# Optimization experiments

Hardware: AMD Instinct MI355X
Metric: run time of the kernel (lower is better)

Reference implementation:

```python
import jax, jax.numpy as jnp
import numpy as np


def setup_inputs() -> dict:
    key = jax.random.key(0)
    ks = jax.random.split(key, 10)
    B, S, I, Hy, H = 16, 4096, 256, 64, 512
    sc = 0.05
    return {
        "x": jax.random.normal(ks[0], (B, S, I), jnp.float32),
        "hidden": jax.random.normal(ks[1], (B, H), jnp.float32),
        "lin0_W": jax.random.normal(ks[2], (Hy, I), jnp.float32) * sc,
        "lin0_b": jax.random.normal(ks[3], (Hy,), jnp.float32) * sc,
        "sig0_W": jax.random.normal(ks[4], (Hy, I), jnp.float32) * sc,
        "sig0_b": jax.random.normal(ks[5], (Hy,), jnp.float32) * sc,
        "fch_W": jax.random.normal(ks[6], (H, Hy), jnp.float32) * sc,
        "fch_b": jax.random.normal(ks[7], (H,), jnp.float32) * sc,
        "fc2_W": jax.random.normal(ks[8], (H, I), jnp.float32) * sc,
        "fc2_b": jax.random.normal(ks[9], (H,), jnp.float32) * sc,
    }


def reference(x, hidden, lin0_W, lin0_b, sig0_W, sig0_b, fch_W, fch_b, fc2_W, fc2_b):
    # GLN sub-network (num_layers=1): relu(linear(x) * sigmoid(linear(x)))
    lin = jnp.einsum('bsi,hi->bsh', x, lin0_W) + lin0_b          # [B,S,Hy]
    gate = jax.nn.sigmoid(jnp.einsum('bsi,hi->bsh', x, sig0_W) + sig0_b)
    g = jax.nn.relu(lin * gate)                                   # [B,S,Hy]
    b = jnp.einsum('bsh,dh->bsd', g, fch_W) + fch_b               # [B,S,H]
    # multihead gating
    sig_alphas = jax.nn.sigmoid(jnp.einsum('bsi,di->bsd', x, fc2_W) + fc2_b)
    b = b * sig_alphas

    # sequential recurrence: h_t = relu(b_t + roll(h_{t-1}, 1, -1)); h_{-1} = hidden
    def step(h, b_t):
        h = jax.nn.relu(b_t + jnp.roll(h, 1, axis=-1))
        return h, h

    b_tmajor = jnp.swapaxes(b, 0, 1)  # [S,B,H]
    last, outs = jax.lax.scan(step, hidden, b_tmajor)
    outputs = jnp.swapaxes(outs, 0, 1)  # [B,S,H]
    return outputs, last
```

## Files before the change

### kernel.cpp

```cpp
#include <hip/hip_runtime.h>

typedef __attribute__((ext_vector_type(4))) float  f32x4;
typedef __attribute__((ext_vector_type(4))) short  s16x4;
typedef __attribute__((ext_vector_type(8))) short  s16x8;
typedef __bf16 bf16x8 __attribute__((ext_vector_type(8)));

#define NBATCH 16
#define SEQ    4096
#define KIN    256
#define HY     64
#define HOUT   512
#define NROWS  (NBATCH*SEQ)
#define LC     32
#define NC     (SEQ/LC)

#define GP(x) ((const __attribute__((address_space(1))) void*)(x))
#define LP(x) ((__attribute__((address_space(3))) void*)(x))

static __device__ __forceinline__ short f2bf(float f) {
  unsigned u = __float_as_uint(f);
  u = u + 0x7FFF + ((u >> 16) & 1);
  return (short)(u >> 16);
}
static __device__ __forceinline__ float bf2f(short h) {
  return __uint_as_float(((unsigned)(unsigned short)h) << 16);
}
static __device__ __forceinline__ f32x4 mfma16(bf16x8 a, bf16x8 b, f32x4 c) {
  return __builtin_amdgcn_mfma_f32_16x16x32_bf16(a, b, c, 0, 0, 0);
}
static __device__ __forceinline__ bf16x8 ldfrag(const short* p) {
  return *reinterpret_cast<const bf16x8*>(p);
}
static __device__ __forceinline__ float fsigmoid(float z) {
  return 1.f / (1.f + __expf(-z));
}

__global__ void prep_w(const float* __restrict__ lin0W, const float* __restrict__ sig0W,
                       const float* __restrict__ fchW,  const float* __restrict__ fc2W,
                       short* __restrict__ W1h, short* __restrict__ W2h,
                       short* __restrict__ Fh,  short* __restrict__ F2h) {
  int i = blockIdx.x * 256 + threadIdx.x;
  if (i < 16384) {
    W1h[i] = f2bf(lin0W[i]);
    W2h[i] = f2bf(sig0W[i]);
  } else if (i < 16384 + 32768) {
    Fh[i - 16384] = f2bf(fchW[i - 16384]);
  } else if (i < 16384 + 32768 + 131072) {
    F2h[i - 49152] = f2bf(fc2W[i - 49152]);
  }
}

__global__ __launch_bounds__(256) void gx(
    const float* __restrict__ x,
    const short* __restrict__ W1h, const short* __restrict__ W2h,
    const float* __restrict__ lin0b, const float* __restrict__ sig0b,
    short* __restrict__ Gh, short* __restrict__ xh) {
  __shared__ __align__(16) short smem[64 * 256 + 64 * 64];
  short* Ah = smem;
  short* gL = smem + 64 * 256;
  int tid = threadIdx.x;
  int row0 = blockIdx.x * 64;
  #pragma unroll
  for (int i = 0; i < 16; ++i) {
    int f4 = tid + i * 256;
    int r = f4 >> 6, k = (f4 & 63) << 2;
    f32x4 v = *reinterpret_cast<const f32x4*>(x + (size_t)(row0 + r) * KIN + k);
    s16x4 hh;
    #pragma unroll
    for (int j = 0; j < 4; ++j) hh[j] = f2bf(v[j]);
    *reinterpret_cast<s16x4*>(&Ah[(r * 256 + k) ^ ((r & 7) << 3)]) = hh;
    *reinterpret_cast<s16x4*>(xh + (size_t)(row0 + r) * KIN + k) = hh;
  }
  __syncthreads();
  int w = tid >> 6, l = tid & 63, lr = l & 15, lg = l >> 4;
  {
    int c = w * 16 + lr;
    f32x4 a1[4], a2[4];
    #pragma unroll
    for (int rt = 0; rt < 4; ++rt) { a1[rt] = (f32x4)0.f; a2[rt] = (f32x4)0.f; }
    #pragma unroll
    for (int ks = 0; ks < 8; ++ks) {
      int kk = ks * 32 + lg * 8;
      bf16x8 b1 = ldfrag(W1h + c * 256 + kk);
      bf16x8 b2 = ldfrag(W2h + c * 256 + kk);
      #pragma unroll
      for (int rt = 0; rt < 4; ++rt) {
        int r = rt * 16 + lr;
        bf16x8 a = ldfrag(&Ah[(r * 256 + kk) ^ ((r & 7) << 3)]);
        a1[rt] = mfma16(b1, a, a1[rt]);
        a2[rt] = mfma16(b2, a, a2[rt]);
      }
    }
    f32x4 blv = *reinterpret_cast<const f32x4*>(lin0b + w * 16 + lg * 4);
    f32x4 bsv = *reinterpret_cast<const f32x4*>(sig0b + w * 16 + lg * 4);
    #pragma unroll
    for (int rt = 0; rt < 4; ++rt) {
      int xrl = rt * 16 + lr;
      s16x4 gg;
      #pragma unroll
      for (int j = 0; j < 4; ++j) {
        float g = (a1[rt][j] + blv[j]) * fsigmoid(a2[rt][j] + bsv[j]);
        gg[j] = f2bf(g > 0.f ? g : 0.f);
      }
      *reinterpret_cast<s16x4*>(&gL[(xrl * 64 + w * 16 + lg * 4) ^ ((xrl & 7) << 3)]) = gg;
    }
  }
  __syncthreads();
  #pragma unroll
  for (int i = 0; i < 2; ++i) {
    int slot = i * 256 + tid;
    int row = slot >> 3, c8 = slot & 7;
    s16x8 v = *reinterpret_cast<const s16x8*>(&gL[(row * 64 + c8 * 8) ^ ((row & 7) << 3)]);
    *reinterpret_cast<s16x8*>(Gh + (size_t)(row0 + row) * HY + c8 * 8) = v;
  }
}

__global__ __launch_bounds__(256) void bg(
    const short* __restrict__ xh, const short* __restrict__ Gh,
    const short* __restrict__ F2h, const short* __restrict__ Fh,
    const float* __restrict__ fchb, const float* __restrict__ fc2b,
    short* __restrict__ Bb) {
  __shared__ __align__(16) short smem[16384];
  short* As = smem;
  short* Bs = smem + 8192;
  short* bT = smem;
  int tid = threadIdx.x;
  int w = tid >> 6, l = tid & 63;
  int lr = l & 15, lg = l >> 4;
  int r0 = (w >> 1) * 64, c0 = (w & 1) * 64;
  int bid = blockIdx.x;
  int v = (bid & 7) * 256 + (bid >> 3);
  int rowTile = v & 511;
  int colTile = v >> 9;
  int row0 = rowTile * 128;
  int col0 = colTile * 128;

  auto stage = [&](int t) {
    #pragma unroll
    for (int j = 0; j < 4; ++j) {
      int flat = (w * 4 + j) * 64 + l;
      int row = flat >> 3, sp = flat & 7;
      int seg = sp ^ (row & 7);
      const short* asrc = (t < 4) ? xh + (size_t)(row0 + row) * KIN + t * 64 + seg * 8
                                  : Gh + (size_t)(row0 + row) * HY + seg * 8;
      const short* bsrc = (t < 4) ? F2h + (size_t)(col0 + row) * KIN + t * 64 + seg * 8
                                  : Fh + (size_t)(col0 + row) * HY + seg * 8;
      __builtin_amdgcn_global_load_lds(GP(asrc), LP(&As[(w * 4 + j) * 512]), 16, 0, 0);
      __builtin_amdgcn_global_load_lds(GP(bsrc), LP(&Bs[(w * 4 + j) * 512]), 16, 0, 0);
    }
  };
  auto compute = [&](f32x4 (&acc)[4][4]) {
    #pragma unroll
    for (int ksl = 0; ksl < 2; ++ksl) {
      bf16x8 Af[4], Bf[4];
      #pragma unroll
      for (int i = 0; i < 4; ++i) {
        int row = r0 + i * 16 + lr;
        Af[i] = ldfrag(&As[row * 64 + ((ksl * 32 + lg * 8) ^ ((row & 7) << 3))]);
        int col = c0 + i * 16 + lr;
        Bf[i] = ldfrag(&Bs[col * 64 + ((ksl * 32 + lg * 8) ^ ((col & 7) << 3))]);
      }
      #pragma unroll
      for (int rt = 0; rt < 4; ++rt)
        #pragma unroll
        for (int ct = 0; ct < 4; ++ct)
          acc[rt][ct] = mfma16(Af[rt], Bf[ct], acc[rt][ct]);
    }
  };

  f32x4 acc2[4][4], accF[4][4];
  #pragma unroll
  for (int rt = 0; rt < 4; ++rt)
    #pragma unroll
    for (int ct = 0; ct < 4; ++ct) { acc2[rt][ct] = (f32x4)0.f; accF[rt][ct] = (f32x4)0.f; }

  #pragma unroll
  for (int t = 0; t < 5; ++t) {
    stage(t);
    __syncthreads();
    if (t < 4) compute(acc2); else compute(accF);
    __syncthreads();
  }

  #pragma unroll
  for (int ct = 0; ct < 4; ++ct) {
    int lc = c0 + ct * 16 + lr;
    int col = col0 + lc;
    float bc = fchb[col], b2c = fc2b[col];
    #pragma unroll
    for (int rt = 0; rt < 4; ++rt) {
      int tl0 = r0 + rt * 16 + lg * 4;
      #pragma unroll
      for (int j = 0; j < 4; ++j) {
        int tl = tl0 + j;
        float alpha = fsigmoid(acc2[rt][ct][j] + b2c);
        bT[(tl * 128 + lc) ^ ((tl & 7) << 3)] = f2bf((accF[rt][ct][j] + bc) * alpha);
      }
    }
  }
  __syncthreads();
  #pragma unroll
  for (int i = 0; i < 8; ++i) {
    int slot = i * 256 + tid;
    int row = slot >> 4, c8 = slot & 15;
    s16x8 vv = *reinterpret_cast<const s16x8*>(&bT[(row * 128 + c8 * 8) ^ ((row & 7) << 3)]);
    *reinterpret_cast<s16x8*>(Bb + (size_t)(row0 + row) * HOUT + col0 + c8 * 8) = vv;
  }
}

__global__ __launch_bounds__(64) void scan_passA(const short* __restrict__ Bb,
                                                 float* __restrict__ Cc, float* __restrict__ Sc) {
  int bc = blockIdx.x;
  int l = threadIdx.x;
  int row0 = bc * LC;
  const short* bp = Bb + (size_t)row0 * HOUT + l * 8;
  s16x8 vc = *reinterpret_cast<const s16x8*>(bp);
  float C[8], S[8];
  #pragma unroll
  for (int i = 0; i < 8; ++i) { S[i] = bf2f(vc[i]); C[i] = 0.f; }
  for (int t = 1; t < LC; ++t) {
    s16x8 vn = *reinterpret_cast<const s16x8*>(bp + (size_t)t * HOUT);
    float bb[8];
    #pragma unroll
    for (int i = 0; i < 8; ++i) bb[i] = bf2f(vn[i]);
    float pC = __shfl(C[7], (l + 63) & 63);
    float pS = __shfl(S[7], (l + 63) & 63);
    #pragma unroll
    for (int i = 7; i >= 1; --i) { C[i] = fmaxf(0.f, bb[i] + C[i - 1]); S[i] = bb[i] + S[i - 1]; }
    C[0] = fmaxf(0.f, bb[0] + pC);
    S[0] = bb[0] + pS;
  }
  float* cp = Cc + (size_t)bc * HOUT + l * 8;
  float* sp = Sc + (size_t)bc * HOUT + l * 8;
  #pragma unroll
  for (int i = 0; i < 8; ++i) { cp[i] = C[i]; sp[i] = S[i]; }
}

__global__ __launch_bounds__(64) void scan_combine(const float* __restrict__ hidden,
                                                   const float* __restrict__ Cc, const float* __restrict__ Sc,
                                                   float* __restrict__ hIn, float* __restrict__ lastOut) {
  int batch = blockIdx.x;
  int l = threadIdx.x;
  float h[8];
  const float* hp = hidden + batch * HOUT + l * 8;
  #pragma unroll
  for (int i = 0; i < 8; ++i) h[i] = hp[i];
  size_t base0 = ((size_t)batch * NC) * HOUT + l * 8;
  f32x4 c0 = *reinterpret_cast<const f32x4*>(Cc + base0);
  f32x4 c1 = *reinterpret_cast<const f32x4*>(Cc + base0 + 4);
  f32x4 s0 = *reinterpret_cast<const f32x4*>(Sc + base0);
  f32x4 s1 = *reinterpret_cast<const f32x4*>(Sc + base0 + 4);
  for (int c = 0; c < NC; ++c) {
    size_t base = base0 + (size_t)c * HOUT;
    f32x4 nc0, nc1, ns0, ns1;
    if (c + 1 < NC) {
      size_t nb = base + HOUT;
      nc0 = *reinterpret_cast<const f32x4*>(Cc + nb);
      nc1 = *reinterpret_cast<const f32x4*>(Cc + nb + 4);
      ns0 = *reinterpret_cast<const f32x4*>(Sc + nb);
      ns1 = *reinterpret_cast<const f32x4*>(Sc + nb + 4);
    }
    #pragma unroll
    for (int i = 0; i < 8; ++i) hIn[base + i] = h[i];
    float hs[8];
    #pragma unroll
    for (int i = 0; i < 8; ++i) hs[i] = __shfl(h[i], (l + 64 - (LC / 8)) & 63);
    #pragma unroll
    for (int i = 0; i < 4; ++i) {
      h[i]     = fmaxf(c0[i], s0[i] + hs[i]);
      h[4 + i] = fmaxf(c1[i], s1[i] + hs[4 + i]);
    }
    c0 = nc0; c1 = nc1; s0 = ns0; s1 = ns1;
  }
  float* lp = lastOut + batch * HOUT + l * 8;
  #pragma unroll
  for (int i = 0; i < 8; ++i) lp[i] = h[i];
}

__global__ __launch_bounds__(64) void scan_passB(const short* __restrict__ bws,
                                                 const float* __restrict__ hIn,
                                                 float* __restrict__ hout) {
  int bc = blockIdx.x;
  int l = threadIdx.x;
  int row0 = bc * LC;
  const float* hp = hIn + (size_t)bc * HOUT + l * 8;
  float h[8];
  #pragma unroll
  for (int i = 0; i < 8; ++i) h[i] = hp[i];
  s16x8 vc = *reinterpret_cast<const s16x8*>(bws + (size_t)row0 * HOUT + l * 8);
  for (int t = 0; t < LC; ++t) {
    s16x8 vn;
    if (t + 1 < LC)
      vn = *reinterpret_cast<const s16x8*>(bws + (size_t)(row0 + t + 1) * HOUT + l * 8);
    float bb[8];
    #pragma unroll
    for (int i = 0; i < 8; ++i) bb[i] = bf2f(vc[i]);
    float ph = __shfl(h[7], (l + 63) & 63);
    #pragma unroll
    for (int i = 7; i >= 1; --i) h[i] = fmaxf(0.f, bb[i] + h[i - 1]);
    h[0] = fmaxf(0.f, bb[0] + ph);
    f32x4 o0, o1;
    #pragma unroll
    for (int i = 0; i < 4; ++i) { o0[i] = h[i]; o1[i] = h[4 + i]; }
    float* bt = hout + (size_t)(row0 + t) * HOUT + l * 8;
    *reinterpret_cast<f32x4*>(bt) = o0;
    *reinterpret_cast<f32x4*>(bt + 4) = o1;
    vc = vn;
  }
}

extern "C" void kernel_launch(void* const* d_in, const int* in_sizes, int n_in,
                              void* d_out, int out_size, void* d_ws, size_t ws_size,
                              hipStream_t stream) {
  (void)in_sizes; (void)n_in; (void)out_size; (void)ws_size;
  const float* x      = (const float*)d_in[0];
  const float* hidden = (const float*)d_in[1];
  const float* lin0W  = (const float*)d_in[2];
  const float* lin0b  = (const float*)d_in[3];
  const float* sig0W  = (const float*)d_in[4];
  const float* sig0b  = (const float*)d_in[5];
  const float* fchW   = (const float*)d_in[6];
  const float* fchb   = (const float*)d_in[7];
  const float* fc2W   = (const float*)d_in[8];
  const float* fc2b   = (const float*)d_in[9];
  float* outO  = (float*)d_out;
  float* lastO = outO + (size_t)NROWS * HOUT;

  char* wsb = (char*)d_ws;
  size_t off = 0;
  auto alloc = [&](size_t bytes) { char* p = wsb + off; off += (bytes + 255) & ~(size_t)255; return p; };
  float* Cc  = (float*)alloc((size_t)NBATCH * NC * HOUT * 4);
  float* Sc  = (float*)alloc((size_t)NBATCH * NC * HOUT * 4);
  float* hIn = (float*)alloc((size_t)NBATCH * NC * HOUT * 4);
  short* W1h = (short*)alloc(HY * KIN * 2);
  short* W2h = (short*)alloc(HY * KIN * 2);
  short* Fh  = (short*)alloc(HOUT * HY * 2);
  short* F2h = (short*)alloc(HOUT * KIN * 2);
  short* Gh  = (short*)alloc((size_t)NROWS * HY * 2);
  short* xh  = (short*)alloc((size_t)NROWS * KIN * 2);
  short* Bb  = (short*)alloc((size_t)NROWS * HOUT * 2);

  prep_w<<<704, 256, 0, stream>>>(lin0W, sig0W, fchW, fc2W, W1h, W2h, Fh, F2h);
  gx<<<NROWS / 64, 256, 0, stream>>>(x, W1h, W2h, lin0b, sig0b, Gh, xh);
  bg<<<2048, 256, 0, stream>>>(xh, Gh, F2h, Fh, fchb, fc2b, Bb);
  scan_passA<<<NBATCH * NC, 64, 0, stream>>>(Bb, Cc, Sc);
  scan_combine<<<NBATCH, 64, 0, stream>>>(hidden, Cc, Sc, hIn, lastO);
  scan_passB<<<NBATCH * NC, 64, 0, stream>>>(Bb, hIn, outO);
}
```

Baseline: 176.2 us.

## Double-buffer bg GEMM LDS stages and split tile across 8 waves

Moves the bg kernel from 4 to 8 waves per 128x128 tile, with each wave now computing a 32x64 sub-tile. It also double-buffers the shared-memory stage so the next K-slice's global-to-LDS loads are issued before the current slice is computed, dropping one barrier per step. The aim is to hide load latency and raise the number of waves available per CU. The cost is double the LDS (64 KB per block), which may limit how many blocks fit per CU. It also relies on the async loads being complete at the barrier that ends the previous iteration.

```diff
diff --git a/kernel.cpp b/kernel.cpp
--- a/kernel.cpp
+++ b/kernel.cpp
@@ -115,19 +115,18 @@
   }
 }
 
-__global__ __launch_bounds__(256) void bg(
+__global__ __launch_bounds__(512, 4) void bg(
     const short* __restrict__ xh, const short* __restrict__ Gh,
     const short* __restrict__ F2h, const short* __restrict__ Fh,
     const float* __restrict__ fchb, const float* __restrict__ fc2b,
     short* __restrict__ Bb) {
-  __shared__ __align__(16) short smem[16384];
-  short* As = smem;
-  short* Bs = smem + 8192;
-  short* bT = smem;
+  __shared__ __align__(16) short smem[2][16384];
+  short* bT = &smem[0][0];
   int tid = threadIdx.x;
   int w = tid >> 6, l = tid & 63;
   int lr = l & 15, lg = l >> 4;
-  int r0 = (w >> 1) * 64, c0 = (w & 1) * 64;
+  int r0 = (w >> 1) * 32;
+  int c0 = (w & 1) * 64;
   int bid = blockIdx.x;
   int v = (bid & 7) * 256 + (bid >> 3);
   int rowTile = v & 511;
@@ -135,50 +134,63 @@
   int row0 = rowTile * 128;
   int col0 = colTile * 128;
 
-  auto stage = [&](int t) {
-    #pragma unroll
-    for (int j = 0; j < 4; ++j) {
-      int flat = (w * 4 + j) * 64 + l;
+  auto stage = [&](int t, int b) {
+    short* As = &smem[b][0];
+    short* Bs = &smem[b][8192];
+    #pragma unroll
+    for (int j = 0; j < 1; ++j) {
+    }
+    #pragma unroll
+    for (int j = 0; j < 2; ++j) {
+      int blk = w * 2 + j;
+      int flat = blk * 64 + l;
       int row = flat >> 3, sp = flat & 7;
       int seg = sp ^ (row & 7);
       const short* asrc = (t < 4) ? xh + (size_t)(row0 + row) * KIN + t * 64 + seg * 8
                                   : Gh + (size_t)(row0 + row) * HY + seg * 8;
       const short* bsrc = (t < 4) ? F2h + (size_t)(col0 + row) * KIN + t * 64 + seg * 8
                                   : Fh + (size_t)(col0 + row) * HY + seg * 8;
-      __builtin_amdgcn_global_load_lds(GP(asrc), LP(&As[(w * 4 + j) * 512]), 16, 0, 0);
-      __builtin_amdgcn_global_load_lds(GP(bsrc), LP(&Bs[(w * 4 + j) * 512]), 16, 0, 0);
+      __builtin_amdgcn_global_load_lds(GP(asrc), LP(&As[blk * 512]), 16, 0, 0);
+      __builtin_amdgcn_global_load_lds(GP(bsrc), LP(&Bs[blk * 512]), 16, 0, 0);
     }
   };
-  auto compute = [&](f32x4 (&acc)[4][4]) {
+  auto compute = [&](int b, f32x4 (&acc)[2][4]) {
+    short* As = &smem[b][0];
+    short* Bs = &smem[b][8192];
     #pragma unroll
     for (int ksl = 0; ksl < 2; ++ksl) {
-      bf16x8 Af[4], Bf[4];
-      #pragma unroll
-      for (int i = 0; i < 4; ++i) {
+      bf16x8 Af[2], Bf[4];
+      #pragma unroll
+      for (int i = 0; i < 2; ++i) {
         int row = r0 + i * 16 + lr;
         Af[i] = ldfrag(&As[row * 64 + ((ksl * 32 + lg * 8) ^ ((row & 7) << 3))]);
+      }
+      #pragma unroll
+      for (int i = 0; i < 4; ++i) {
         int col = c0 + i * 16 + lr;
         Bf[i] = ldfrag(&Bs[col * 64 + ((ksl * 32 + lg * 8) ^ ((col & 7) << 3))]);
       }
       #pragma unroll
-      for (int rt = 0; rt < 4; ++rt)
+      for (int rt = 0; rt < 2; ++rt)
         #pragma unroll
         for (int ct = 0; ct < 4; ++ct)
           acc[rt][ct] = mfma16(Af[rt], Bf[ct], acc[rt][ct]);
     }
   };
 
-  f32x4 acc2[4][4], accF[4][4];
-  #pragma unroll
-  for (int rt = 0; rt < 4; ++rt)
+  f32x4 acc2[2][4], accF[2][4];
+  #pragma unroll
+  for (int rt = 0; rt < 2; ++rt)
     #pragma unroll
     for (int ct = 0; ct < 4; ++ct) { acc2[rt][ct] = (f32x4)0.f; accF[rt][ct] = (f32x4)0.f; }
 
+  stage(0, 0);
+  __syncthreads();
   #pragma unroll
   for (int t = 0; t < 5; ++t) {
-    stage(t);
-    __syncthreads();
-    if (t < 4) compute(acc2); else compute(accF);
+    if (t < 4) stage(t + 1, (t + 1) & 1);
+    if (t < 4) compute(t & 1, acc2);
+    else       compute(t & 1, accF);
     __syncthreads();
   }
 
@@ -188,7 +200,7 @@
     int col = col0 + lc;
     float bc = fchb[col], b2c = fc2b[col];
     #pragma unroll
-    for (int rt = 0; rt < 4; ++rt) {
+    for (int rt = 0; rt < 2; ++rt) {
       int tl0 = r0 + rt * 16 + lg * 4;
       #pragma unroll
       for (int j = 0; j < 4; ++j) {
@@ -200,8 +212,8 @@
   }
   __syncthreads();
   #pragma unroll
-  for (int i = 0; i < 8; ++i) {
-    int slot = i * 256 + tid;
+  for (int i = 0; i < 4; ++i) {
+    int slot = i * 512 + tid;
     int row = slot >> 4, c8 = slot & 15;
     s16x8 vv = *reinterpret_cast<const s16x8*>(&bT[(row * 128 + c8 * 8) ^ ((row & 7) << 3)]);
     *reinterpret_cast<s16x8*>(Bb + (size_t)(row0 + row) * HOUT + col0 + c8 * 8) = vv;
@@ -342,7 +354,7 @@
 
   prep_w<<<704, 256, 0, stream>>>(lin0W, sig0W, fchW, fc2W, W1h, W2h, Fh, F2h);
   gx<<<NROWS / 64, 256, 0, stream>>>(x, W1h, W2h, lin0b, sig0b, Gh, xh);
-  bg<<<2048, 256, 0, stream>>>(xh, Gh, F2h, Fh, fchb, fc2b, Bb);
+  bg<<<2048, 512, 0, stream>>>(xh, Gh, F2h, Fh, fchb, fc2b, Bb);
   scan_passA<<<NBATCH * NC, 64, 0, stream>>>(Bb, Cc, Sc);
   scan_combine<<<NBATCH, 64, 0, stream>>>(hidden, Cc, Sc, hIn, lastO);
   scan_passB<<<NBATCH * NC, 64, 0, stream>>>(Bb, hIn, outO);
```

New measurement: 178.7 us. No clear change (+1.4%).
